# Kernel optimization log

Measured on AMD Instinct MI355X. Metric: run time of the kernel, lower is better.

Reference implementation:

```python
import jax, jax.numpy as jnp
import numpy as np

B, T, D = 8, 4096, 512
Q, K = 4, 1024
KERNEL, STRIDE = 5, 2
COMMIT = 0.25


def setup_inputs() -> dict:
    key = jax.random.key(0)
    k1, k2, k3 = jax.random.split(key, 3)
    x = jax.random.normal(k1, (B, T, D), dtype=jnp.float32)
    codebooks = jax.random.normal(k2, (Q, K, D), dtype=jnp.float32)
    # he_normal fan_in = KERNEL * D
    conv_w = jax.random.normal(k3, (KERNEL, D, D), dtype=jnp.float32) * np.sqrt(2.0 / (KERNEL * D))
    return {"x": x, "codebooks": codebooks, "conv_w": conv_w}


def _vq_nearest(residual, cb):
    # residual: [B,T,D], cb: [K,D] -> squared L2 distances [B,T,K]
    d = (jnp.sum(residual * residual, axis=-1, keepdims=True)
         - 2.0 * jnp.einsum('btd,kd->btk', residual, cb)
         + jnp.sum(cb * cb, axis=-1))
    idx = jnp.argmin(d, axis=-1)          # [B,T] int
    q = cb[idx]                            # [B,T,D] gather
    return q, idx


def residual_vq(x, codebooks):
    residual = x
    quantized_out = jnp.zeros_like(x)
    losses = []
    indices = []
    for qi in range(Q):  # small fixed number of quantizers
        q, idx = _vq_nearest(residual, codebooks[qi])
        # commitment loss (codebook frozen at inference / EMA-updated in training)
        losses.append(COMMIT * jnp.mean((jax.lax.stop_gradient(q) - residual) ** 2))
        # straight-through estimator
        q_st = residual + jax.lax.stop_gradient(q - residual)
        quantized_out = quantized_out + q_st
        residual = residual - jax.lax.stop_gradient(q)
        indices.append(idx)
    loss = jnp.sum(jnp.stack(losses))
    return quantized_out, jnp.stack(indices, axis=0), loss


def reference(x, codebooks, conv_w):
    quantized_out, indices, vq_loss = residual_vq(x, codebooks)
    # Conv1D, stride 2, 'same' padding, no bias: NWC x WIO -> NWC
    y = jax.lax.conv_general_dilated(
        quantized_out, conv_w,
        window_strides=(STRIDE,), padding='SAME',
        dimension_numbers=('NWC', 'WIO', 'NWC'))
    y = jax.nn.gelu(y, approximate=False)
    return y, quantized_out, indices, vq_loss
```

## Files before the change

### kernel.cpp

```cpp
#include <hip/hip_runtime.h>
#include <math.h>

#define Bq 8
#define Tq 4096
#define Dq 512
#define Qn 4
#define Kk 1024
#define OWn 2048
#define NROWS (Bq*Tq)

#define QO_OFF (Bq*OWn*Dq)
#define IDX_OFF (QO_OFF + Bq*Tq*Dq)
#define LOSS_OFF (IDX_OFF + Qn*NROWS)

typedef __bf16 bf16x8 __attribute__((ext_vector_type(8)));
typedef _Float16 f16x8 __attribute__((ext_vector_type(8)));
typedef float f32x16 __attribute__((ext_vector_type(16)));
typedef float f32x4 __attribute__((ext_vector_type(4)));

__device__ __forceinline__ unsigned pack2h(_Float16 a, _Float16 b) {
  return (unsigned)__builtin_bit_cast(unsigned short, a)
       | ((unsigned)__builtin_bit_cast(unsigned short, b) << 16);
}
__device__ __forceinline__ unsigned pmin2h(unsigned a, unsigned b) {
  _Float16 al = __builtin_bit_cast(_Float16, (unsigned short)(a & 0xFFFFu));
  _Float16 ah = __builtin_bit_cast(_Float16, (unsigned short)(a >> 16));
  _Float16 bl = __builtin_bit_cast(_Float16, (unsigned short)(b & 0xFFFFu));
  _Float16 bh = __builtin_bit_cast(_Float16, (unsigned short)(b >> 16));
  _Float16 ml = al < bl ? al : bl;
  _Float16 mh = ah < bh ? ah : bh;
  return pack2h(ml, mh);
}

__global__ __launch_bounds__(256) void prep_cb(const float* __restrict__ cb,
                                               float* __restrict__ cbnorm,
                                               _Float16* __restrict__ cbf,
                                               float* __restrict__ lacc) {
  int w = threadIdx.x >> 6, lane = threadIdx.x & 63;
  int row = blockIdx.x * 4 + w;
  int q = row >> 10, k = row & 1023;
  const f32x4* c4 = (const f32x4*)(cb + (size_t)row * Dq);
  f32x4 v0 = c4[lane * 2], v1 = c4[lane * 2 + 1];
  float s = v0.x*v0.x + v0.y*v0.y + v0.z*v0.z + v0.w*v0.w
          + v1.x*v1.x + v1.y*v1.y + v1.z*v1.z + v1.w*v1.w;
  f16x8 bv;
  bv[0]=(_Float16)v0.x; bv[1]=(_Float16)v0.y; bv[2]=(_Float16)v0.z; bv[3]=(_Float16)v0.w;
  bv[4]=(_Float16)v1.x; bv[5]=(_Float16)v1.y; bv[6]=(_Float16)v1.z; bv[7]=(_Float16)v1.w;
  int ds = lane >> 1, hs = lane & 1;
  size_t off = ((size_t)((k >> 5) * 32 + ds) * 2 + hs) * 256 + (k & 31) * 8;
  *(f16x8*)(cbf + (size_t)q * (Kk * Dq) + off) = bv;
#pragma unroll
  for (int off2 = 32; off2; off2 >>= 1) s += __shfl_down(s, off2);
  if (lane == 0) cbnorm[row] = s;
  if (blockIdx.x == 0 && threadIdx.x == 0) *lacc = 0.f;
}

__global__ __launch_bounds__(256) void prep_cmax(const float* __restrict__ cbnorm,
                                                 float* __restrict__ cmax) {
  int w = threadIdx.x >> 6, lane = threadIdx.x & 63;
  float m = 0.f;
#pragma unroll
  for (int j = 0; j < 16; ++j) m = fmaxf(m, cbnorm[w * Kk + lane * 16 + j]);
#pragma unroll
  for (int off = 32; off; off >>= 1) m = fmaxf(m, __shfl_down(m, off));
  if (lane == 0) cmax[w] = sqrtf(m);
}

__global__ __launch_bounds__(256) void prep_wb(const float* __restrict__ w,
                                               __bf16* __restrict__ wb) {
  int g = blockIdx.x * 256 + threadIdx.x;
  int l31 = g & 31, hs = (g >> 5) & 1, c32 = (g >> 6) & 15, s = g >> 10;
  int kw = s >> 5, ci16 = s & 31;
  int ci = ci16 * 16 + hs * 8;
  int co = c32 * 32 + l31;
  bf16x8 bv;
#pragma unroll
  for (int e = 0; e < 8; ++e)
    bv[e] = (__bf16)w[(size_t)(kw * Dq + ci + e) * Dq + co];
  *(bf16x8*)(wb + (size_t)g * 8) = bv;
}

__global__ __launch_bounds__(512, 1) void vq_all(
    const float* __restrict__ x, float* __restrict__ qo,
    const _Float16* __restrict__ cbf, const float* __restrict__ cb,
    const float* __restrict__ cbnorm, const float* __restrict__ cmax,
    float* __restrict__ idxo, float* __restrict__ lacc) {
  __shared__ _Float16 rh[64 * 512];
  __shared__ float minW[64 * 8];
  __shared__ float rnorm_l[64];
  __shared__ float thrL[64];
  __shared__ int rowcount[64];
  __shared__ unsigned short rowlist[64 * 32];

  const int tid = threadIdx.x;
  const int w = tid >> 6, lane = tid & 63, l31 = lane & 31, hs = lane >> 5;
  const int row0g = blockIdx.x * 64;
  char* rhc = (char*)rh;

  f32x4 r0[8], r1[8];
#pragma unroll
  for (int rr = 0; rr < 8; ++rr) {
    size_t gb = (size_t)(row0g + w * 8 + rr) * Dq + lane * 8;
    r0[rr] = *(const f32x4*)(x + gb);
    r1[rr] = *(const f32x4*)(x + gb + 4);
  }
  float lsum = 0.f;

#pragma unroll 1
  for (int qi = 0; qi < Qn; ++qi) {
    const _Float16* cbf_q = cbf + (size_t)qi * (Kk * Dq);
    const float*    cb_q  = cb  + (size_t)qi * (Kk * Dq);
    const float*    cbn_q = cbnorm + qi * Kk;

#pragma unroll
    for (int rr = 0; rr < 8; ++rr) {
      int row = w * 8 + rr;
      f16x8 bv;
      bv[0]=(_Float16)r0[rr].x; bv[1]=(_Float16)r0[rr].y;
      bv[2]=(_Float16)r0[rr].z; bv[3]=(_Float16)r0[rr].w;
      bv[4]=(_Float16)r1[rr].x; bv[5]=(_Float16)r1[rr].y;
      bv[6]=(_Float16)r1[rr].z; bv[7]=(_Float16)r1[rr].w;
      *(f16x8*)(rhc + ((row * 1024 + lane * 16) ^ ((row & 7) << 4))) = bv;
      float rn = r0[rr].x*r0[rr].x + r0[rr].y*r0[rr].y + r0[rr].z*r0[rr].z + r0[rr].w*r0[rr].w
               + r1[rr].x*r1[rr].x + r1[rr].y*r1[rr].y + r1[rr].z*r1[rr].z + r1[rr].w*r1[rr].w;
#pragma unroll
      for (int off = 1; off < 64; off <<= 1) rn += __shfl_xor(rn, off);
      if (lane == 0) rnorm_l[row] = rn;
    }
    __syncthreads();

    const int ab0 = l31 * 1024 + hs * 16;
    const int ab1 = ab0 + 32 * 1024;
    const int asw = (l31 & 7) << 4;

    unsigned minp[16];
#pragma unroll
    for (int i = 0; i < 16; ++i) minp[i] = 0x7C007C00u;

#pragma unroll 1
    for (int ct = 0; ct < 4; ++ct) {
      const int col = w * 128 + ct * 32 + l31;
      const _Float16* bp = cbf_q + (size_t)(w * 4 + ct) * 16384 + hs * 256 + l31 * 8;
      f32x16 acc0, acc1;
#pragma unroll
      for (int i = 0; i < 16; ++i) { acc0[i] = 0.f; acc1[i] = 0.f; }
#pragma unroll 8
      for (int ds = 0; ds < 32; ++ds) {
        f16x8 a0 = *(const f16x8*)(rhc + ((ab0 + ds * 32) ^ asw));
        f16x8 a1 = *(const f16x8*)(rhc + ((ab1 + ds * 32) ^ asw));
        f16x8 b  = *(const f16x8*)(bp + ds * 512);
        acc0 = __builtin_amdgcn_mfma_f32_32x32x16_f16(a0, b, acc0, 0, 0, 0);
        acc1 = __builtin_amdgcn_mfma_f32_32x32x16_f16(a1, b, acc1, 0, 0, 0);
      }
      const float cn = cbn_q[col];
#pragma unroll
      for (int i = 0; i < 16; ++i) {
        _Float16 h0 = (_Float16)(cn - 2.f * acc0[i]);
        _Float16 h1 = (_Float16)(cn - 2.f * acc1[i]);
        minp[i] = pmin2h(minp[i], pack2h(h0, h1));
      }
    }
#pragma unroll
    for (int i = 0; i < 16; ++i) {
#pragma unroll
      for (int off = 1; off <= 16; off <<= 1)
        minp[i] = pmin2h(minp[i], __shfl_xor(minp[i], off));
    }
    if (l31 == 0) {
#pragma unroll
      for (int i = 0; i < 16; ++i) {
        int rit = (i & 3) + 8 * (i >> 2) + 4 * hs;
        minW[rit * 8 + w] =
            (float)__builtin_bit_cast(_Float16, (unsigned short)(minp[i] & 0xFFFFu));
        minW[(rit + 32) * 8 + w] =
            (float)__builtin_bit_cast(_Float16, (unsigned short)(minp[i] >> 16));
      }
    }
    __syncthreads();

    if (tid < 64) {
      float m = minW[tid * 8];
#pragma unroll
      for (int j = 1; j < 8; ++j) m = fminf(m, minW[tid * 8 + j]);
      float rn = sqrtf(rnorm_l[tid]);
      float cm = cmax[qi];
      thrL[tid] = m + 0.005f * rn * cm + 0.001f * fabsf(m) + 0.3f;
      rowcount[tid] = 0;
    }
    __syncthreads();

#pragma unroll 1
    for (int ct = 0; ct < 4; ++ct) {
      const int col = w * 128 + ct * 32 + l31;
      const _Float16* bp = cbf_q + (size_t)(w * 4 + ct) * 16384 + hs * 256 + l31 * 8;
      f32x16 acc0, acc1;
#pragma unroll
      for (int i = 0; i < 16; ++i) { acc0[i] = 0.f; acc1[i] = 0.f; }
#pragma unroll 8
      for (int ds = 0; ds < 32; ++ds) {
        f16x8 a0 = *(const f16x8*)(rhc + ((ab0 + ds * 32) ^ asw));
        f16x8 a1 = *(const f16x8*)(rhc + ((ab1 + ds * 32) ^ asw));
        f16x8 b  = *(const f16x8*)(bp + ds * 512);
        acc0 = __builtin_amdgcn_mfma_f32_32x32x16_f16(a0, b, acc0, 0, 0, 0);
        acc1 = __builtin_amdgcn_mfma_f32_32x32x16_f16(a1, b, acc1, 0, 0, 0);
      }
      const float cn = cbn_q[col];
#pragma unroll
      for (int i = 0; i < 16; ++i) {
        int rit = (i & 3) + 8 * (i >> 2) + 4 * hs;
        float s0 = cn - 2.f * acc0[i];
        float s1 = cn - 2.f * acc1[i];
        if (s0 <= thrL[rit]) {
          int p = atomicAdd(&rowcount[rit], 1);
          if (p < 32) rowlist[rit * 32 + p] = (unsigned short)col;
        }
        if (s1 <= thrL[rit + 32]) {
          int p = atomicAdd(&rowcount[rit + 32], 1);
          if (p < 32) rowlist[(rit + 32) * 32 + p] = (unsigned short)col;
        }
      }
    }
    __syncthreads();

#pragma unroll
    for (int rr = 0; rr < 8; ++rr) {
      int row = w * 8 + rr;
      int cnt = rowcount[row];
      int bk;
      if (cnt == 1) {
        bk = (int)rowlist[row * 32];
      } else {
        int total = (cnt > 32) ? Kk : cnt;
        float bs = 3.4028235e38f; bk = 1 << 30;
        for (int ci2 = 0; ci2 < total; ++ci2) {
          int k = (cnt > 32) ? ci2 : (int)rowlist[row * 32 + ci2];
          const f32x4* crow = (const f32x4*)(cb_q + ((size_t)k << 9)) + lane * 2;
          f32x4 c0 = crow[0], c1 = crow[1];
          float dot = 0.f;
          dot = fmaf(r0[rr].x, c0.x, dot); dot = fmaf(r0[rr].y, c0.y, dot);
          dot = fmaf(r0[rr].z, c0.z, dot); dot = fmaf(r0[rr].w, c0.w, dot);
          dot = fmaf(r1[rr].x, c1.x, dot); dot = fmaf(r1[rr].y, c1.y, dot);
          dot = fmaf(r1[rr].z, c1.z, dot); dot = fmaf(r1[rr].w, c1.w, dot);
#pragma unroll
          for (int off = 1; off < 64; off <<= 1) dot += __shfl_xor(dot, off);
          float sc = cbn_q[k] - 2.f * dot;
          if (sc < bs || (sc == bs && k < bk)) { bs = sc; bk = k; }
        }
      }
      if (lane == 0) idxo[(size_t)qi * NROWS + row0g + row] = (float)bk;
      const f32x4* crow = (const f32x4*)(cb_q + ((size_t)bk << 9)) + lane * 2;
      f32x4 c0 = crow[0], c1 = crow[1];
      r0[rr].x -= c0.x; r0[rr].y -= c0.y; r0[rr].z -= c0.z; r0[rr].w -= c0.w;
      r1[rr].x -= c1.x; r1[rr].y -= c1.y; r1[rr].z -= c1.z; r1[rr].w -= c1.w;
      lsum += r0[rr].x*r0[rr].x + r0[rr].y*r0[rr].y + r0[rr].z*r0[rr].z + r0[rr].w*r0[rr].w
            + r1[rr].x*r1[rr].x + r1[rr].y*r1[rr].y + r1[rr].z*r1[rr].z + r1[rr].w*r1[rr].w;
    }
    __syncthreads();
  }

#pragma unroll
  for (int rr = 0; rr < 8; ++rr) {
    size_t gb = (size_t)(row0g + w * 8 + rr) * Dq + lane * 8;
    f32x4 xv0 = *(const f32x4*)(x + gb), xv1 = *(const f32x4*)(x + gb + 4);
    f32x4 o0, o1;
    o0.x = xv0.x - r0[rr].x; o0.y = xv0.y - r0[rr].y;
    o0.z = xv0.z - r0[rr].z; o0.w = xv0.w - r0[rr].w;
    o1.x = xv1.x - r1[rr].x; o1.y = xv1.y - r1[rr].y;
    o1.z = xv1.z - r1[rr].z; o1.w = xv1.w - r1[rr].w;
    *(f32x4*)(qo + gb) = o0;
    *(f32x4*)(qo + gb + 4) = o1;
  }
#pragma unroll
  for (int off = 1; off < 64; off <<= 1) lsum += __shfl_xor(lsum, off);
  if (lane == 0) atomicAdd(lacc, lsum);
}

__global__ __launch_bounds__(512, 2) void conv_mfma(const float* __restrict__ qo,
                                                    const __bf16* __restrict__ wb,
                                                    float* __restrict__ y) {
  __shared__ char As[259 * 128];
  const int tid = threadIdx.x;
  const int w = tid >> 6, lane = tid & 63, l31 = lane & 31, hs = lane >> 5;
  const int rowblk = blockIdx.x, coblk = blockIdx.y;
  const int n = rowblk >> 4;
  const int o0 = (rowblk & 15) * 128;
  const int t0 = 2 * o0 - 1;
  const int c32g = coblk * 8 + w;

  f32x16 acc[4];
#pragma unroll
  for (int rt = 0; rt < 4; ++rt)
#pragma unroll
    for (int i = 0; i < 16; ++i) acc[rt][i] = 0.f;

  for (int ct8 = 0; ct8 < 8; ++ct8) {
    __syncthreads();
    for (int s = tid; s < 2072; s += 512) {
      int irow = s >> 3, cg = s & 7;
      int t = t0 + irow;
      bf16x8 bv;
      if (t >= 0 && t < Tq) {
        const float* src = qo + ((size_t)(n * Tq + t)) * Dq + ct8 * 64 + cg * 8;
        f32x4 v0 = *(const f32x4*)(src), v1 = *(const f32x4*)(src + 4);
        bv[0]=(__bf16)v0.x; bv[1]=(__bf16)v0.y; bv[2]=(__bf16)v0.z; bv[3]=(__bf16)v0.w;
        bv[4]=(__bf16)v1.x; bv[5]=(__bf16)v1.y; bv[6]=(__bf16)v1.z; bv[7]=(__bf16)v1.w;
      } else {
#pragma unroll
        for (int e = 0; e < 8; ++e) bv[e] = (__bf16)0.f;
      }
      *(bf16x8*)(As + ((irow * 128 + cg * 16) ^ (((irow >> 1) & 7) << 4))) = bv;
    }
    __syncthreads();
#pragma unroll
    for (int kw = 0; kw < 5; ++kw) {
#pragma unroll
      for (int ks = 0; ks < 4; ++ks) {
        int s16 = kw * 32 + ct8 * 4 + ks;
        bf16x8 b = *(const bf16x8*)(wb + ((size_t)(s16 * 16 + c32g) * 2 + hs) * 256 + l31 * 8);
#pragma unroll
        for (int rt = 0; rt < 4; ++rt) {
          int ir = 2 * (rt * 32 + l31) + kw;
          bf16x8 a = *(const bf16x8*)(As + ((ir * 128 + ks * 32 + hs * 16) ^ (((ir >> 1) & 7) << 4)));
          acc[rt] = __builtin_amdgcn_mfma_f32_32x32x16_bf16(a, b, acc[rt], 0, 0, 0);
        }
      }
    }
  }
  const int co = coblk * 256 + w * 32 + l31;
#pragma unroll
  for (int rt = 0; rt < 4; ++rt)
#pragma unroll
    for (int i = 0; i < 16; ++i) {
      int orow = rt * 32 + (i & 3) + 8 * (i >> 2) + 4 * hs;
      float v = acc[rt][i];
      float g = 0.5f * v * (1.f + erff(v * 0.70710678118654752f));
      y[((size_t)(n * OWn + o0 + orow)) * Dq + co] = g;
    }
}

__global__ void loss_final(const float* __restrict__ lacc, float* __restrict__ out) {
  out[0] = 0.25f * lacc[0] / 16777216.0f;
}

extern "C" void kernel_launch(void* const* d_in, const int* in_sizes, int n_in,
                              void* d_out, int out_size, void* d_ws, size_t ws_size,
                              hipStream_t stream) {
  const float* x  = (const float*)d_in[0];
  const float* cb = (const float*)d_in[1];
  const float* cw = (const float*)d_in[2];
  float* out = (float*)d_out;
  float* y    = out;
  float* qo   = out + QO_OFF;
  float* idxo = out + IDX_OFF;
  float* losso = out + LOSS_OFF;

  float* fws    = (float*)d_ws;
  float* lacc   = fws;
  float* cmax   = fws + 8;
  float* cbnorm = fws + 16;
  _Float16* cbf = (_Float16*)((char*)d_ws + (32 << 10));
  __bf16* wb  = (__bf16*)((char*)d_ws + (8 << 20));

  prep_cb<<<1024, 256, 0, stream>>>(cb, cbnorm, cbf, lacc);
  prep_cmax<<<1, 256, 0, stream>>>(cbnorm, cmax);
  prep_wb<<<640, 256, 0, stream>>>(cw, wb);

  vq_all<<<512, 512, 0, stream>>>(x, qo, cbf, cb, cbnorm, cmax, idxo, lacc);

  conv_mfma<<<dim3(128, 2), 512, 0, stream>>>(qo, wb, y);
  loss_final<<<1, 1, 0, stream>>>(lacc, losso);
}
```

Measured before the change: 531.5 us.

## Halve VQ block to 4 waves, each computing a 64x64 codebook tile per step

The VQ kernel now runs 256 threads (4 waves) per block instead of 512. Each wave covers 256 codebook columns and 16 rows, computing two 32-column B tiles at once with four MFMA accumulators. Each A fragment read from LDS now feeds two MFMAs instead of one, so LDS reads per MFMA drop. The cost is more registers per thread (64 residual f32x4 vectors plus 64 accumulator floats) and half as many waves per CU, which reduces latency hiding and adds spill risk.

```diff
diff --git a/kernel.cpp b/kernel.cpp
--- a/kernel.cpp
+++ b/kernel.cpp
@@ -80,13 +80,13 @@
   *(bf16x8*)(wb + (size_t)g * 8) = bv;
 }
 
-__global__ __launch_bounds__(512, 1) void vq_all(
+__global__ __launch_bounds__(256, 1) void vq_all(
     const float* __restrict__ x, float* __restrict__ qo,
     const _Float16* __restrict__ cbf, const float* __restrict__ cb,
     const float* __restrict__ cbnorm, const float* __restrict__ cmax,
     float* __restrict__ idxo, float* __restrict__ lacc) {
   __shared__ _Float16 rh[64 * 512];
-  __shared__ float minW[64 * 8];
+  __shared__ float minW[64 * 4];
   __shared__ float rnorm_l[64];
   __shared__ float thrL[64];
   __shared__ int rowcount[64];
@@ -97,10 +97,10 @@
   const int row0g = blockIdx.x * 64;
   char* rhc = (char*)rh;
 
-  f32x4 r0[8], r1[8];
-#pragma unroll
-  for (int rr = 0; rr < 8; ++rr) {
-    size_t gb = (size_t)(row0g + w * 8 + rr) * Dq + lane * 8;
+  f32x4 r0[16], r1[16];
+#pragma unroll
+  for (int rr = 0; rr < 16; ++rr) {
+    size_t gb = (size_t)(row0g + w * 16 + rr) * Dq + lane * 8;
     r0[rr] = *(const f32x4*)(x + gb);
     r1[rr] = *(const f32x4*)(x + gb + 4);
   }
@@ -113,8 +113,8 @@
     const float*    cbn_q = cbnorm + qi * Kk;
 
 #pragma unroll
-    for (int rr = 0; rr < 8; ++rr) {
-      int row = w * 8 + rr;
+    for (int rr = 0; rr < 16; ++rr) {
+      int row = w * 16 + rr;
       f16x8 bv;
       bv[0]=(_Float16)r0[rr].x; bv[1]=(_Float16)r0[rr].y;
       bv[2]=(_Float16)r0[rr].z; bv[3]=(_Float16)r0[rr].w;
@@ -138,26 +138,34 @@
     for (int i = 0; i < 16; ++i) minp[i] = 0x7C007C00u;
 
 #pragma unroll 1
-    for (int ct = 0; ct < 4; ++ct) {
-      const int col = w * 128 + ct * 32 + l31;
-      const _Float16* bp = cbf_q + (size_t)(w * 4 + ct) * 16384 + hs * 256 + l31 * 8;
-      f32x16 acc0, acc1;
-#pragma unroll
-      for (int i = 0; i < 16; ++i) { acc0[i] = 0.f; acc1[i] = 0.f; }
+    for (int p = 0; p < 4; ++p) {
+      const _Float16* bp0 = cbf_q + (size_t)(w * 8 + 2 * p) * 16384 + hs * 256 + l31 * 8;
+      const _Float16* bp1 = bp0 + 16384;
+      f32x16 a00, a01, a10, a11;
+#pragma unroll
+      for (int i = 0; i < 16; ++i) { a00[i]=0.f; a01[i]=0.f; a10[i]=0.f; a11[i]=0.f; }
 #pragma unroll 8
       for (int ds = 0; ds < 32; ++ds) {
         f16x8 a0 = *(const f16x8*)(rhc + ((ab0 + ds * 32) ^ asw));
         f16x8 a1 = *(const f16x8*)(rhc + ((ab1 + ds * 32) ^ asw));
-        f16x8 b  = *(const f16x8*)(bp + ds * 512);
-        acc0 = __builtin_amdgcn_mfma_f32_32x32x16_f16(a0, b, acc0, 0, 0, 0);
-        acc1 = __builtin_amdgcn_mfma_f32_32x32x16_f16(a1, b, acc1, 0, 0, 0);
-      }
-      const float cn = cbn_q[col];
+        f16x8 b0 = *(const f16x8*)(bp0 + ds * 512);
+        f16x8 b1 = *(const f16x8*)(bp1 + ds * 512);
+        a00 = __builtin_amdgcn_mfma_f32_32x32x16_f16(a0, b0, a00, 0, 0, 0);
+        a01 = __builtin_amdgcn_mfma_f32_32x32x16_f16(a0, b1, a01, 0, 0, 0);
+        a10 = __builtin_amdgcn_mfma_f32_32x32x16_f16(a1, b0, a10, 0, 0, 0);
+        a11 = __builtin_amdgcn_mfma_f32_32x32x16_f16(a1, b1, a11, 0, 0, 0);
+      }
+      const float cn0 = cbn_q[w * 256 + 2 * p * 32 + l31];
+      const float cn1 = cbn_q[w * 256 + 2 * p * 32 + 32 + l31];
 #pragma unroll
       for (int i = 0; i < 16; ++i) {
-        _Float16 h0 = (_Float16)(cn - 2.f * acc0[i]);
-        _Float16 h1 = (_Float16)(cn - 2.f * acc1[i]);
-        minp[i] = pmin2h(minp[i], pack2h(h0, h1));
+        _Float16 h00 = (_Float16)(cn0 - 2.f * a00[i]);
+        _Float16 h01 = (_Float16)(cn1 - 2.f * a01[i]);
+        _Float16 h10 = (_Float16)(cn0 - 2.f * a10[i]);
+        _Float16 h11 = (_Float16)(cn1 - 2.f * a11[i]);
+        _Float16 m0 = h00 < h01 ? h00 : h01;
+        _Float16 m1 = h10 < h11 ? h10 : h11;
+        minp[i] = pmin2h(minp[i], pack2h(m0, m1));
       }
     }
 #pragma unroll
@@ -170,18 +178,18 @@
 #pragma unroll
       for (int i = 0; i < 16; ++i) {
         int rit = (i & 3) + 8 * (i >> 2) + 4 * hs;
-        minW[rit * 8 + w] =
+        minW[rit * 4 + w] =
             (float)__builtin_bit_cast(_Float16, (unsigned short)(minp[i] & 0xFFFFu));
-        minW[(rit + 32) * 8 + w] =
+        minW[(rit + 32) * 4 + w] =
             (float)__builtin_bit_cast(_Float16, (unsigned short)(minp[i] >> 16));
       }
     }
     __syncthreads();
 
     if (tid < 64) {
-      float m = minW[tid * 8];
-#pragma unroll
-      for (int j = 1; j < 8; ++j) m = fminf(m, minW[tid * 8 + j]);
+      float m = minW[tid * 4];
+#pragma unroll
+      for (int j = 1; j < 4; ++j) m = fminf(m, minW[tid * 4 + j]);
       float rn = sqrtf(rnorm_l[tid]);
       float cm = cmax[qi];
       thrL[tid] = m + 0.005f * rn * cm + 0.001f * fabsf(m) + 0.3f;
@@ -190,41 +198,58 @@
     __syncthreads();
 
 #pragma unroll 1
-    for (int ct = 0; ct < 4; ++ct) {
-      const int col = w * 128 + ct * 32 + l31;
-      const _Float16* bp = cbf_q + (size_t)(w * 4 + ct) * 16384 + hs * 256 + l31 * 8;
-      f32x16 acc0, acc1;
-#pragma unroll
-      for (int i = 0; i < 16; ++i) { acc0[i] = 0.f; acc1[i] = 0.f; }
+    for (int p = 0; p < 4; ++p) {
+      const _Float16* bp0 = cbf_q + (size_t)(w * 8 + 2 * p) * 16384 + hs * 256 + l31 * 8;
+      const _Float16* bp1 = bp0 + 16384;
+      f32x16 a00, a01, a10, a11;
+#pragma unroll
+      for (int i = 0; i < 16; ++i) { a00[i]=0.f; a01[i]=0.f; a10[i]=0.f; a11[i]=0.f; }
 #pragma unroll 8
       for (int ds = 0; ds < 32; ++ds) {
         f16x8 a0 = *(const f16x8*)(rhc + ((ab0 + ds * 32) ^ asw));
         f16x8 a1 = *(const f16x8*)(rhc + ((ab1 + ds * 32) ^ asw));
-        f16x8 b  = *(const f16x8*)(bp + ds * 512);
-        acc0 = __builtin_amdgcn_mfma_f32_32x32x16_f16(a0, b, acc0, 0, 0, 0);
-        acc1 = __builtin_amdgcn_mfma_f32_32x32x16_f16(a1, b, acc1, 0, 0, 0);
-      }
-      const float cn = cbn_q[col];
+        f16x8 b0 = *(const f16x8*)(bp0 + ds * 512);
+        f16x8 b1 = *(const f16x8*)(bp1 + ds * 512);
+        a00 = __builtin_amdgcn_mfma_f32_32x32x16_f16(a0, b0, a00, 0, 0, 0);
+        a01 = __builtin_amdgcn_mfma_f32_32x32x16_f16(a0, b1, a01, 0, 0, 0);
+        a10 = __builtin_amdgcn_mfma_f32_32x32x16_f16(a1, b0, a10, 0, 0, 0);
+        a11 = __builtin_amdgcn_mfma_f32_32x32x16_f16(a1, b1, a11, 0, 0, 0);
+      }
+      const float cn0 = cbn_q[w * 256 + 2 * p * 32 + l31];
+      const float cn1 = cbn_q[w * 256 + 2 * p * 32 + 32 + l31];
+      const unsigned col0 = (unsigned)(w * 256 + 2 * p * 32 + l31);
+      const unsigned col1 = col0 + 32;
 #pragma unroll
       for (int i = 0; i < 16; ++i) {
         int rit = (i & 3) + 8 * (i >> 2) + 4 * hs;
-        float s0 = cn - 2.f * acc0[i];
-        float s1 = cn - 2.f * acc1[i];
-        if (s0 <= thrL[rit]) {
-          int p = atomicAdd(&rowcount[rit], 1);
-          if (p < 32) rowlist[rit * 32 + p] = (unsigned short)col;
-        }
-        if (s1 <= thrL[rit + 32]) {
-          int p = atomicAdd(&rowcount[rit + 32], 1);
-          if (p < 32) rowlist[(rit + 32) * 32 + p] = (unsigned short)col;
-        }
-      }
-    }
-    __syncthreads();
-
-#pragma unroll
-    for (int rr = 0; rr < 8; ++rr) {
-      int row = w * 8 + rr;
+        float t0 = thrL[rit], t1 = thrL[rit + 32];
+        float s00 = cn0 - 2.f * a00[i];
+        float s01 = cn1 - 2.f * a01[i];
+        float s10 = cn0 - 2.f * a10[i];
+        float s11 = cn1 - 2.f * a11[i];
+        if (s00 <= t0) {
+          int pp = atomicAdd(&rowcount[rit], 1);
+          if (pp < 32) rowlist[rit * 32 + pp] = (unsigned short)col0;
+        }
+        if (s01 <= t0) {
+          int pp = atomicAdd(&rowcount[rit], 1);
+          if (pp < 32) rowlist[rit * 32 + pp] = (unsigned short)col1;
+        }
+        if (s10 <= t1) {
+          int pp = atomicAdd(&rowcount[rit + 32], 1);
+          if (pp < 32) rowlist[(rit + 32) * 32 + pp] = (unsigned short)col0;
+        }
+        if (s11 <= t1) {
+          int pp = atomicAdd(&rowcount[rit + 32], 1);
+          if (pp < 32) rowlist[(rit + 32) * 32 + pp] = (unsigned short)col1;
+        }
+      }
+    }
+    __syncthreads();
+
+#pragma unroll
+    for (int rr = 0; rr < 16; ++rr) {
+      int row = w * 16 + rr;
       int cnt = rowcount[row];
       int bk;
       if (cnt == 1) {
@@ -259,8 +284,8 @@
   }
 
 #pragma unroll
-  for (int rr = 0; rr < 8; ++rr) {
-    size_t gb = (size_t)(row0g + w * 8 + rr) * Dq + lane * 8;
+  for (int rr = 0; rr < 16; ++rr) {
+    size_t gb = (size_t)(row0g + w * 16 + rr) * Dq + lane * 8;
     f32x4 xv0 = *(const f32x4*)(x + gb), xv1 = *(const f32x4*)(x + gb + 4);
     f32x4 o0, o1;
     o0.x = xv0.x - r0[rr].x; o0.y = xv0.y - r0[rr].y;
@@ -365,7 +390,7 @@
   prep_cmax<<<1, 256, 0, stream>>>(cbnorm, cmax);
   prep_wb<<<640, 256, 0, stream>>>(cw, wb);
 
-  vq_all<<<512, 512, 0, stream>>>(x, qo, cbf, cb, cbnorm, cmax, idxo, lacc);
+  vq_all<<<512, 256, 0, stream>>>(x, qo, cbf, cb, cbnorm, cmax, idxo, lacc);
 
   conv_mfma<<<dim3(128, 2), 512, 0, stream>>>(qo, wb, y);
   loss_final<<<1, 1, 0, stream>>>(lacc, losso);
```

New measurement: 673.8 us. +26.8%, slower.
